# Kernel tuning notes

Hardware: AMD Instinct MI355X
Metric: run time of the kernel (lower is better)

Reference implementation:

```python
import jax, jax.numpy as jnp
import numpy as np

T, B, D, H, O = 512, 64, 1024, 1024, 1024
N_LAYERS = 2


def setup_inputs() -> dict:
    key = jax.random.key(0)
    ks = jax.random.split(key, 1 + 4 * N_LAYERS)
    inp = {
        "x": jax.random.normal(ks[0], (T, B, D), dtype=jnp.float32),
        "paddings": jnp.zeros((T, B, 1), dtype=jnp.float32),
    }
    d_in = D
    for i in range(N_LAYERS):
        s_ih = 1.0 / np.sqrt(d_in)
        s_hh = 1.0 / np.sqrt(H)
        inp[f"Wih{i}"] = jax.random.normal(ks[1 + 4 * i], (d_in, 3 * H), jnp.float32) * s_ih
        inp[f"Whh{i}"] = jax.random.normal(ks[2 + 4 * i], (H, 3 * H), jnp.float32) * s_hh
        inp[f"b{i}"] = jnp.zeros((3 * H,), jnp.float32)
        inp[f"Who{i}"] = jax.random.normal(ks[3 + 4 * i], (H, O), jnp.float32) * s_hh
        d_in = O
    return inp


def _gru_layer(x, p, Wih, Whh, b, Who):
    # x: [T, B, D_in], p: [T, B, 1]
    Bsz = x.shape[1]
    Hd = Whh.shape[0]
    # precompute input-side gates for all steps: [T, B, 3H]
    gx_all = jnp.einsum("tbd,dk->tbk", x, Wih) + b

    def step(h, inp):
        gx, pt = inp  # gx: [B, 3H], pt: [B, 1]
        gh = h @ Whh  # [B, 3H]
        r = jax.nn.sigmoid(gx[:, :Hd] + gh[:, :Hd])
        z = jax.nn.sigmoid(gx[:, Hd:2 * Hd] + gh[:, Hd:2 * Hd])
        n = jnp.tanh(gx[:, 2 * Hd:] + r * gh[:, 2 * Hd:])
        h_new = (1.0 - z) * n + z * h
        h_new = pt * h + (1.0 - pt) * h_new  # padded steps keep state
        return h_new, h_new

    h0 = jnp.zeros((Bsz, Hd), x.dtype)
    _, hs = jax.lax.scan(step, h0, (gx_all, p))  # hs: [T, B, H]
    return jnp.einsum("tbh,ho->tbo", hs, Who)


def reference(x, paddings, Wih0, Whh0, b0, Who0, Wih1, Whh1, b1, Who1):
    layers = [(Wih0, Whh0, b0, Who0), (Wih1, Whh1, b1, Who1)]
    xs = x
    for (Wih, Whh, b, Who) in layers:
        xs = _gru_layer(xs, paddings, Wih, Whh, b, Who)
    return xs
```

## Files before the change

kernel.cpp:

```cpp
#include <hip/hip_runtime.h>
#include <hip/hip_bf16.h>

typedef __bf16 bf16;
typedef __bf16 bf16x8 __attribute__((ext_vector_type(8)));
typedef float  f32x4  __attribute__((ext_vector_type(4)));
typedef unsigned long long u64;
typedef unsigned short u16;

__global__ __launch_bounds__(256) void cast_f32_bf16(const float* __restrict__ in,
                                                     bf16* __restrict__ out) {
    size_t i = ((size_t)blockIdx.x * blockDim.x + threadIdx.x) * 8;
    float4 a = *(const float4*)(in + i);
    float4 b = *(const float4*)(in + i + 4);
    bf16x8 o;
    o[0] = (bf16)a.x; o[1] = (bf16)a.y; o[2] = (bf16)a.z; o[3] = (bf16)a.w;
    o[4] = (bf16)b.x; o[5] = (bf16)b.y; o[6] = (bf16)b.z; o[7] = (bf16)b.w;
    *(bf16x8*)(out + i) = o;
}

__global__ __launch_bounds__(256) void transpose_cast(const float* __restrict__ in,
                                                      bf16* __restrict__ out,
                                                      int R, int C) {
    __shared__ float tile[32][33];
    int c0 = blockIdx.x * 32, r0 = blockIdx.y * 32;
    int tx = threadIdx.x & 31, ty = threadIdx.x >> 5;
    #pragma unroll
    for (int i = 0; i < 32; i += 8)
        tile[ty + i][tx] = in[(size_t)(r0 + ty + i) * C + c0 + tx];
    __syncthreads();
    #pragma unroll
    for (int i = 0; i < 32; i += 8)
        out[(size_t)(c0 + ty + i) * R + r0 + tx] = (bf16)tile[tx][ty + i];
}

template<bool BF16_OUT, bool HAS_BIAS>
__global__ __launch_bounds__(256) void gemm128(const bf16* __restrict__ A,
                                               const bf16* __restrict__ Bt,
                                               const float* __restrict__ bias,
                                               void* __restrict__ Cout,
                                               int M, int N, int K) {
    __shared__ bf16 sA[128][72];
    __shared__ bf16 sB[128][72];
    const int tid = threadIdx.x, lane = tid & 63, w = tid >> 6;
    const int wr = w >> 1, wc = w & 1;
    const int m0 = blockIdx.y * 128, n0 = blockIdx.x * 128;
    const int ml = lane & 15, kb = (lane >> 4) * 8;

    f32x4 acc[4][4] = {};
    const bf16* Ab = A  + (size_t)m0 * K;
    const bf16* Bb = Bt + (size_t)n0 * K;

    for (int kc = 0; kc < K; kc += 64) {
        #pragma unroll
        for (int i = 0; i < 4; ++i) {
            int c = tid + 256 * i;
            int row = c >> 3, col = (c & 7) * 8;
            *(uint4*)&sA[row][col] = *(const uint4*)(Ab + (size_t)row * K + kc + col);
            *(uint4*)&sB[row][col] = *(const uint4*)(Bb + (size_t)row * K + kc + col);
        }
        __syncthreads();
        #pragma unroll
        for (int ks = 0; ks < 2; ++ks) {
            bf16x8 af[4], bfr[4];
            #pragma unroll
            for (int i = 0; i < 4; ++i)
                af[i] = *(const bf16x8*)&sA[wr * 64 + i * 16 + ml][ks * 32 + kb];
            #pragma unroll
            for (int i = 0; i < 4; ++i)
                bfr[i] = *(const bf16x8*)&sB[wc * 64 + i * 16 + ml][ks * 32 + kb];
            #pragma unroll
            for (int mi = 0; mi < 4; ++mi)
                #pragma unroll
                for (int ni = 0; ni < 4; ++ni)
                    acc[mi][ni] = __builtin_amdgcn_mfma_f32_16x16x32_bf16(
                        af[mi], bfr[ni], acc[mi][ni], 0, 0, 0);
        }
        __syncthreads();
    }
    const int rbase = (lane >> 4) * 4;
    #pragma unroll
    for (int mi = 0; mi < 4; ++mi) {
        #pragma unroll
        for (int ni = 0; ni < 4; ++ni) {
            int col = n0 + wc * 64 + ni * 16 + ml;
            float bv = HAS_BIAS ? bias[col] : 0.f;
            #pragma unroll
            for (int r = 0; r < 4; ++r) {
                int row = m0 + wr * 64 + mi * 16 + rbase + r;
                float v = acc[mi][ni][r] + bv;
                if constexpr (BF16_OUT)
                    ((bf16*)Cout)[(size_t)row * N + col] = (bf16)v;
                else
                    ((float*)Cout)[(size_t)row * N + col] = v;
            }
        }
    }
}

__device__ __forceinline__ void mm_step(const char* sW, const char* hslot,
                                        int wv, int lane, int kb, int ml,
                                        f32x4 acc[3]) {
    const char* rowp = hslot + wv * 32768 + (lane >> 4) * 256 + ml * 16;
    uint4 hq[32];
    #pragma unroll
    for (int ks = 0; ks < 32; ++ks)
        asm volatile("global_load_dwordx4 %0, %1, off"
                     : "=v"(hq[ks]) : "v"(rowp + ks * 1024) : "memory");
    asm volatile("s_waitcnt vmcnt(16)" ::: "memory");
    __builtin_amdgcn_sched_barrier(0);
    #pragma unroll
    for (int ks = 0; ks < 16; ++ks) {
        bf16x8 af = __builtin_bit_cast(bf16x8, hq[ks]);
        #pragma unroll
        for (int g = 0; g < 3; ++g) {
            int brow = g * 16 + ml;
            int addr = brow * 2048 + (ks * 32 + kb) * 2;
            addr ^= (brow & 7) << 4;
            bf16x8 bw = *(const bf16x8*)(sW + addr);
            acc[g] = __builtin_amdgcn_mfma_f32_16x16x32_bf16(af, bw, acc[g], 0, 0, 0);
        }
    }
    asm volatile("s_waitcnt vmcnt(0)" ::: "memory");
    __builtin_amdgcn_sched_barrier(0);
    #pragma unroll
    for (int ks = 16; ks < 32; ++ks) {
        bf16x8 af = __builtin_bit_cast(bf16x8, hq[ks]);
        #pragma unroll
        for (int g = 0; g < 3; ++g) {
            int brow = g * 16 + ml;
            int addr = brow * 2048 + (ks * 32 + kb) * 2;
            addr ^= (brow & 7) << 4;
            bf16x8 bw = *(const bf16x8*)(sW + addr);
            acc[g] = __builtin_amdgcn_mfma_f32_16x16x32_bf16(af, bw, acc[g], 0, 0, 0);
        }
    }
}

__device__ __forceinline__ void store_pair_frag(char* slot, int b, int j,
                                                unsigned short v, int ml) {
    unsigned nb = (unsigned)__shfl_xor((int)(unsigned)v, 1, 64);
    if ((ml & 1) == 0) {
        unsigned pk = (unsigned)v | (nb << 16);
        size_t off = (size_t)((b >> 4) * 32768 + (j >> 5) * 1024 +
                              ((j >> 3) & 3) * 256 + (b & 15) * 16 + (j & 7) * 2);
        __hip_atomic_store((unsigned*)(slot + off), pk,
                           __ATOMIC_RELAXED, __HIP_MEMORY_SCOPE_AGENT);
    }
}

__device__ __forceinline__ void poll1(const u16* a, unsigned ta, int lane) {
    while (true) {
        unsigned fa = (unsigned)__hip_atomic_load(a + lane, __ATOMIC_RELAXED,
                                                  __HIP_MEMORY_SCOPE_AGENT);
        if (__all((int)(fa >= ta))) break;
        __builtin_amdgcn_s_sleep(8);
    }
    asm volatile("" ::: "memory");
}

__device__ __forceinline__ void publish1(u16* s1, unsigned val, int lane) {
    asm volatile("s_waitcnt vmcnt(0)" ::: "memory");
    if (lane == 0)
        __hip_atomic_store(s1, (u16)val, __ATOMIC_RELAXED, __HIP_MEMORY_SCOPE_AGENT);
}
__device__ __forceinline__ void publish2(u16* s1, u16* s2, unsigned val, int lane) {
    asm volatile("s_waitcnt vmcnt(0)" ::: "memory");
    if (lane == 0) {
        __hip_atomic_store(s1, (u16)val, __ATOMIC_RELAXED, __HIP_MEMORY_SCOPE_AGENT);
        __hip_atomic_store(s2, (u16)val, __ATOMIC_RELAXED, __HIP_MEMORY_SCOPE_AGENT);
    }
}

__global__ __launch_bounds__(256, 1) void gru_fused(
    const bf16* __restrict__ WH1T, const bf16* __restrict__ W2fT,
    const bf16* __restrict__ WH2T, const bf16* __restrict__ gx1,
    const float* __restrict__ pad, const float* __restrict__ b2,
    char* __restrict__ h1f,
    bf16* __restrict__ gx2ring,
    char* __restrict__ hs2f,
    bf16* __restrict__ hs2row,
    u16* __restrict__ f1s, u16* __restrict__ f1c,
    u16* __restrict__ f2,
    u16* __restrict__ f3s, u16* __restrict__ f3c) {
    extern __shared__ __align__(16) char sW[];

    const int tid = threadIdx.x, lane = tid & 63, wv = tid >> 6;
    const int role = blockIdx.x >> 6, jg = blockIdx.x & 63;
    const int j0 = jg * 16;
    const int ml = lane & 15, kb = (lane >> 4) * 8;
    const int rbase = (lane >> 4) * 4;
    const int bbase = wv * 16 + rbase;
    const int jml = j0 + ml;

    const bf16* Wsrc = (role == 0) ? WH1T : (role == 1) ? W2fT : WH2T;
    #pragma unroll 1
    for (int i = 0; i < 24; ++i) {
        int c = tid + 256 * i;
        int rr = c >> 7;
        int off = (c & 127) * 16;
        int gate = rr >> 4, j = rr & 15;
        const bf16* src = Wsrc + (size_t)(gate * 1024 + j0 + j) * 1024 + off / 2;
        *(uint4*)(sW + rr * 2048 + (off ^ ((rr & 7) << 4))) = *(const uint4*)src;
    }
    __syncthreads();

    if (role == 0) {
        u16* fown = f1s + wv * 64;
        float hreg[4] = {0.f, 0.f, 0.f, 0.f};
        float gxv[12]; float4 pv;
        #pragma unroll
        for (int r = 0; r < 4; ++r) {
            size_t b = (size_t)(bbase + r);
            gxv[r * 3 + 0] = (float)gx1[b * 3072 + jml];
            gxv[r * 3 + 1] = (float)gx1[b * 3072 + 1024 + jml];
            gxv[r * 3 + 2] = (float)gx1[b * 3072 + 2048 + jml];
        }
        pv = *(const float4*)(pad + bbase);

        for (int t = 0; t < 512; ++t) {
            f32x4 acc[3] = {};
            if (t > 0) {
                poll1(fown, (unsigned)t, lane);
                mm_step(sW, h1f + (size_t)(t - 1) * 131072, wv, lane, kb, ml, acc);
            }
            unsigned short hpk[4];
            #pragma unroll
            for (int r = 0; r < 4; ++r) {
                float rr = 1.f / (1.f + __expf(-(gxv[r * 3 + 0] + acc[0][r])));
                float zz = 1.f / (1.f + __expf(-(gxv[r * 3 + 1] + acc[1][r])));
                float nn = tanhf(gxv[r * 3 + 2] + rr * acc[2][r]);
                float hold = hreg[r];
                float hn = (1.f - zz) * nn + zz * hold;
                float p = (r == 0) ? pv.x : (r == 1) ? pv.y : (r == 2) ? pv.z : pv.w;
                hn = p * hold + (1.f - p) * hn;
                hreg[r] = hn;
                hpk[r] = __builtin_bit_cast(unsigned short, (bf16)hn);
            }
            char* hst = h1f + (size_t)t * 131072;
            #pragma unroll
            for (int r = 0; r < 4; ++r)
                store_pair_frag(hst, bbase + r, jml, hpk[r], ml);
            publish2(fown + jg, f1c + wv * 64 + jg, (unsigned)(t + 1), lane);
            {
                int tn = (t < 511) ? t + 1 : 511;
                const bf16* gxt = gx1 + (size_t)tn * 64 * 3072;
                #pragma unroll
                for (int r = 0; r < 4; ++r) {
                    size_t b = (size_t)(bbase + r);
                    gxv[r * 3 + 0] = (float)gxt[b * 3072 + jml];
                    gxv[r * 3 + 1] = (float)gxt[b * 3072 + 1024 + jml];
                    gxv[r * 3 + 2] = (float)gxt[b * 3072 + 2048 + jml];
                }
                pv = *(const float4*)(pad + tn * 64 + bbase);
            }
        }
    } else if (role == 1) {
        u16* fsrc = f1c + wv * 64;
        u16* fbp  = f3c + wv * 64;
        for (int t = 0; t < 512; ++t) {
            poll1(fsrc, (unsigned)(t + 1), lane);
            f32x4 acc[3] = {};
            mm_step(sW, h1f + (size_t)t * 131072, wv, lane, kb, ml, acc);
            if (t >= 16)
                poll1(fbp, (unsigned)(t - 15), lane);
            bf16* dst = gx2ring + (size_t)(t & 15) * 196608;
            #pragma unroll
            for (int g = 0; g < 3; ++g) {
                unsigned short w0 = __builtin_bit_cast(unsigned short, (bf16)acc[g][0]);
                unsigned short w1 = __builtin_bit_cast(unsigned short, (bf16)acc[g][1]);
                unsigned short w2 = __builtin_bit_cast(unsigned short, (bf16)acc[g][2]);
                unsigned short w3 = __builtin_bit_cast(unsigned short, (bf16)acc[g][3]);
                u64 pk = (u64)w0 | ((u64)w1 << 16) | ((u64)w2 << 32) | ((u64)w3 << 48);
                __hip_atomic_store((u64*)(dst + ((size_t)(g * 1024 + jml)) * 64 + bbase),
                                   pk, __ATOMIC_RELAXED, __HIP_MEMORY_SCOPE_AGENT);
            }
            publish1(f2 + wv * 64 + jg, (unsigned)(t + 1), lane);
        }
    } else {
        u16* fown = f3s + wv * 64;
        u16* fgx  = f2 + wv * 64;
        float b2v[3] = {b2[jml], b2[1024 + jml], b2[2048 + jml]};
        float hreg[4] = {0.f, 0.f, 0.f, 0.f};
        float4 pv = *(const float4*)(pad + bbase);

        for (int t = 0; t < 512; ++t) {
            poll1(fgx, (unsigned)(t + 1), lane);
            const bf16* gsl = gx2ring + (size_t)(t & 15) * 196608;
            u64 gq[3];
            #pragma unroll
            for (int g = 0; g < 3; ++g)
                gq[g] = __hip_atomic_load(
                    (const u64*)(gsl + ((size_t)(g * 1024 + jml)) * 64 + bbase),
                    __ATOMIC_RELAXED, __HIP_MEMORY_SCOPE_AGENT);
            f32x4 acc[3] = {};
            if (t > 0) {
                poll1(fown, (unsigned)t, lane);
                mm_step(sW, hs2f + (size_t)((t - 1) & 15) * 131072, wv, lane, kb, ml, acc);
            }
            unsigned short hpk[4];
            #pragma unroll
            for (int r = 0; r < 4; ++r) {
                float gr = (float)__builtin_bit_cast(bf16,
                    (unsigned short)(gq[0] >> (r * 16))) + b2v[0];
                float gz = (float)__builtin_bit_cast(bf16,
                    (unsigned short)(gq[1] >> (r * 16))) + b2v[1];
                float gn = (float)__builtin_bit_cast(bf16,
                    (unsigned short)(gq[2] >> (r * 16))) + b2v[2];
                float rr = 1.f / (1.f + __expf(-(gr + acc[0][r])));
                float zz = 1.f / (1.f + __expf(-(gz + acc[1][r])));
                float nn = tanhf(gn + rr * acc[2][r]);
                float hold = hreg[r];
                float hn = (1.f - zz) * nn + zz * hold;
                float p = (r == 0) ? pv.x : (r == 1) ? pv.y : (r == 2) ? pv.z : pv.w;
                hn = p * hold + (1.f - p) * hn;
                hreg[r] = hn;
                hpk[r] = __builtin_bit_cast(unsigned short, (bf16)hn);
            }
            char* hstf = hs2f + (size_t)(t & 15) * 131072;
            #pragma unroll
            for (int r = 0; r < 4; ++r)
                store_pair_frag(hstf, bbase + r, jml, hpk[r], ml);
            bf16* hstr = hs2row + (size_t)t * 65536;
            #pragma unroll
            for (int r = 0; r < 4; ++r) {
                unsigned nb = (unsigned)__shfl_xor((int)(unsigned)hpk[r], 1, 64);
                if ((ml & 1) == 0) {
                    unsigned pk = (unsigned)hpk[r] | (nb << 16);
                    *(unsigned*)(hstr + (size_t)(bbase + r) * 1024 + jml) = pk;
                }
            }
            publish2(fown + jg, f3c + wv * 64 + jg, (unsigned)(t + 1), lane);
            int tn = (t < 511) ? t + 1 : 511;
            pv = *(const float4*)(pad + tn * 64 + bbase);
        }
    }
}

extern "C" void kernel_launch(void* const* d_in, const int* in_sizes, int n_in,
                              void* d_out, int out_size, void* d_ws, size_t ws_size,
                              hipStream_t stream) {
    const float* x    = (const float*)d_in[0];
    const float* pad  = (const float*)d_in[1];
    const float* Wih1 = (const float*)d_in[2];
    const float* Whh1 = (const float*)d_in[3];
    const float* b1   = (const float*)d_in[4];
    const float* Who1 = (const float*)d_in[5];
    const float* Wih2 = (const float*)d_in[6];
    const float* Whh2 = (const float*)d_in[7];
    const float* b2   = (const float*)d_in[8];
    const float* Who2 = (const float*)d_in[9];
    float* out_f = (float*)d_out;

    char* p = (char*)d_ws;
    bf16* xb      = (bf16*)p; p += (size_t)32768 * 1024 * 2;
    bf16* gxb     = (bf16*)p; p += (size_t)32768 * 3072 * 2;
    char* h1f     = p;        p += (size_t)512 * 131072;
    bf16* hs2row  = (bf16*)p; p += (size_t)32768 * 1024 * 2;
    char* hs2f    = p;        p += (size_t)16 * 131072;
    bf16* gx2ring = (bf16*)p; p += (size_t)16 * 196608 * 2;
    bf16* WT1     = (bf16*)p; p += (size_t)3072 * 1024 * 2;
    bf16* who1b   = (bf16*)p; p += (size_t)1024 * 1024 * 2;
    bf16* W2fT    = (bf16*)p; p += (size_t)3072 * 1024 * 2;
    bf16* WH1     = (bf16*)p; p += (size_t)3072 * 1024 * 2;
    bf16* WH2     = (bf16*)p; p += (size_t)3072 * 1024 * 2;
    u16* flags = (u16*)p; p += 8192;
    u16* f1s = flags,        * f1c = flags + 256;
    u16* f2  = flags + 512;
    u16* f3s = flags + 768,  * f3c = flags + 1024;

    hipFuncSetAttribute((const void*)gru_fused,
                        hipFuncAttributeMaxDynamicSharedMemorySize, 131072);

    cast_f32_bf16<<<16384, 256, 0, stream>>>(x, xb);
    transpose_cast<<<dim3(96, 32), 256, 0, stream>>>(Wih1, WT1, 1024, 3072);
    gemm128<true, true><<<dim3(24, 256), 256, 0, stream>>>(
        xb, WT1, b1, gxb, 32768, 3072, 1024);
    transpose_cast<<<dim3(96, 32), 256, 0, stream>>>(Wih2, WT1, 1024, 3072);
    cast_f32_bf16<<<512, 256, 0, stream>>>(Who1, who1b);
    gemm128<true, false><<<dim3(8, 24), 256, 0, stream>>>(
        WT1, who1b, nullptr, W2fT, 3072, 1024, 1024);
    transpose_cast<<<dim3(96, 32), 256, 0, stream>>>(Whh1, WH1, 1024, 3072);
    transpose_cast<<<dim3(96, 32), 256, 0, stream>>>(Whh2, WH2, 1024, 3072);
    transpose_cast<<<dim3(32, 32), 256, 0, stream>>>(Who2, WT1, 1024, 1024);
    hipMemsetAsync(flags, 0, 8192, stream);
    gru_fused<<<192, 256, 98304, stream>>>(WH1, W2fT, WH2, gxb, pad, b2,
                                           h1f, gx2ring, hs2f, hs2row,
                                           f1s, f1c, f2, f3s, f3c);
    gemm128<false, false><<<dim3(8, 256), 256, 0, stream>>>(
        hs2row, WT1, nullptr, out_f, 32768, 1024, 1024);
}
```

Before: 4.763 ms.

## Split role-1 projection GEMM along K into two halves with wider column tiles

The role-1 blocks, which compute the layer-2 input gates from layer-1 hidden states, now each cover 32 columns over half of K instead of 16 columns over all of K. Each block loads only half of the h slice per step (16 loads instead of 32) and issues 6 MFMA accumulators per k-step, which should shorten per-step latency on the critical pipeline. The two K-halves write separate partial sums into a ring buffer of twice the size, and the role-2 consumer loads both halves and adds them. This doubles gx2 ring traffic and rounds each partial sum to bf16 before the add, which slightly changes precision.

New measurement: 4.950 ms. +3.9%, slower.

```diff
diff --git a/kernel.cpp b/kernel.cpp
--- a/kernel.cpp
+++ b/kernel.cpp
@@ -97,6 +97,7 @@
     }
 }
 
+
 __device__ __forceinline__ void mm_step(const char* sW, const char* hslot,
                                         int wv, int lane, int kb, int ml,
                                         f32x4 acc[3]) {
@@ -133,6 +134,47 @@
             bf16x8 bw = *(const bf16x8*)(sW + addr);
             acc[g] = __builtin_amdgcn_mfma_f32_16x16x32_bf16(af, bw, acc[g], 0, 0, 0);
         }
+    }
+}
+
+__device__ __forceinline__ void mm_step16(const char* sW, const char* hslot,
+                                          int kh, int wv, int lane, int kb, int ml,
+                                          f32x4 acc[3][2]) {
+    const char* rowp = hslot + wv * 32768 + (lane >> 4) * 256 + ml * 16 + kh * 16384;
+    uint4 hq[16];
+    #pragma unroll
+    for (int ks = 0; ks < 16; ++ks)
+        asm volatile("global_load_dwordx4 %0, %1, off"
+                     : "=v"(hq[ks]) : "v"(rowp + ks * 1024) : "memory");
+    asm volatile("s_waitcnt vmcnt(8)" ::: "memory");
+    __builtin_amdgcn_sched_barrier(0);
+    #pragma unroll
+    for (int ks = 0; ks < 8; ++ks) {
+        bf16x8 af = __builtin_bit_cast(bf16x8, hq[ks]);
+        #pragma unroll
+        for (int g = 0; g < 3; ++g)
+            #pragma unroll
+            for (int ct = 0; ct < 2; ++ct) {
+                int brow = g * 32 + ct * 16 + ml;
+                int addr = brow * 1024 + (((ks * 32 + kb) * 2) ^ ((brow & 7) << 4));
+                bf16x8 bw = *(const bf16x8*)(sW + addr);
+                acc[g][ct] = __builtin_amdgcn_mfma_f32_16x16x32_bf16(af, bw, acc[g][ct], 0, 0, 0);
+            }
+    }
+    asm volatile("s_waitcnt vmcnt(0)" ::: "memory");
+    __builtin_amdgcn_sched_barrier(0);
+    #pragma unroll
+    for (int ks = 8; ks < 16; ++ks) {
+        bf16x8 af = __builtin_bit_cast(bf16x8, hq[ks]);
+        #pragma unroll
+        for (int g = 0; g < 3; ++g)
+            #pragma unroll
+            for (int ct = 0; ct < 2; ++ct) {
+                int brow = g * 32 + ct * 16 + ml;
+                int addr = brow * 1024 + (((ks * 32 + kb) * 2) ^ ((brow & 7) << 4));
+                bf16x8 bw = *(const bf16x8*)(sW + addr);
+                acc[g][ct] = __builtin_amdgcn_mfma_f32_16x16x32_bf16(af, bw, acc[g][ct], 0, 0, 0);
+            }
     }
 }
 
@@ -192,15 +234,29 @@
     const int bbase = wv * 16 + rbase;
     const int jml = j0 + ml;
 
-    const bf16* Wsrc = (role == 0) ? WH1T : (role == 1) ? W2fT : WH2T;
-    #pragma unroll 1
-    for (int i = 0; i < 24; ++i) {
-        int c = tid + 256 * i;
-        int rr = c >> 7;
-        int off = (c & 127) * 16;
-        int gate = rr >> 4, j = rr & 15;
-        const bf16* src = Wsrc + (size_t)(gate * 1024 + j0 + j) * 1024 + off / 2;
-        *(uint4*)(sW + rr * 2048 + (off ^ ((rr & 7) << 4))) = *(const uint4*)src;
+    if (role == 1) {
+        const int cgrp = jg >> 1, kh = jg & 1;
+        #pragma unroll 1
+        for (int i = 0; i < 24; ++i) {
+            int c = tid + 256 * i;
+            int row = c >> 6;
+            int off = (c & 63) * 16;
+            int gate = row >> 5, cx = row & 31;
+            const bf16* src = W2fT + (size_t)(gate * 1024 + cgrp * 32 + cx) * 1024
+                              + kh * 512 + off / 2;
+            *(uint4*)(sW + row * 1024 + (off ^ ((row & 7) << 4))) = *(const uint4*)src;
+        }
+    } else {
+        const bf16* Wsrc = (role == 0) ? WH1T : WH2T;
+        #pragma unroll 1
+        for (int i = 0; i < 24; ++i) {
+            int c = tid + 256 * i;
+            int rr = c >> 7;
+            int off = (c & 127) * 16;
+            int gate = rr >> 4, j = rr & 15;
+            const bf16* src = Wsrc + (size_t)(gate * 1024 + j0 + j) * 1024 + off / 2;
+            *(uint4*)(sW + rr * 2048 + (off ^ ((rr & 7) << 4))) = *(const uint4*)src;
+        }
     }
     __syncthreads();
 
@@ -255,25 +311,29 @@
             }
         }
     } else if (role == 1) {
+        const int cgrp = jg >> 1, kh = jg & 1;
         u16* fsrc = f1c + wv * 64;
         u16* fbp  = f3c + wv * 64;
         for (int t = 0; t < 512; ++t) {
             poll1(fsrc, (unsigned)(t + 1), lane);
-            f32x4 acc[3] = {};
-            mm_step(sW, h1f + (size_t)t * 131072, wv, lane, kb, ml, acc);
+            f32x4 acc2[3][2] = {};
+            mm_step16(sW, h1f + (size_t)t * 131072, kh, wv, lane, kb, ml, acc2);
             if (t >= 16)
                 poll1(fbp, (unsigned)(t - 15), lane);
-            bf16* dst = gx2ring + (size_t)(t & 15) * 196608;
-            #pragma unroll
-            for (int g = 0; g < 3; ++g) {
-                unsigned short w0 = __builtin_bit_cast(unsigned short, (bf16)acc[g][0]);
-                unsigned short w1 = __builtin_bit_cast(unsigned short, (bf16)acc[g][1]);
-                unsigned short w2 = __builtin_bit_cast(unsigned short, (bf16)acc[g][2]);
-                unsigned short w3 = __builtin_bit_cast(unsigned short, (bf16)acc[g][3]);
-                u64 pk = (u64)w0 | ((u64)w1 << 16) | ((u64)w2 << 32) | ((u64)w3 << 48);
-                __hip_atomic_store((u64*)(dst + ((size_t)(g * 1024 + jml)) * 64 + bbase),
-                                   pk, __ATOMIC_RELAXED, __HIP_MEMORY_SCOPE_AGENT);
-            }
+            bf16* dst = gx2ring + (size_t)(t & 15) * 393216 + (size_t)kh * 196608;
+            #pragma unroll
+            for (int g = 0; g < 3; ++g)
+                #pragma unroll
+                for (int ct = 0; ct < 2; ++ct) {
+                    int col = cgrp * 32 + ct * 16 + ml;
+                    unsigned short w0 = __builtin_bit_cast(unsigned short, (bf16)acc2[g][ct][0]);
+                    unsigned short w1 = __builtin_bit_cast(unsigned short, (bf16)acc2[g][ct][1]);
+                    unsigned short w2 = __builtin_bit_cast(unsigned short, (bf16)acc2[g][ct][2]);
+                    unsigned short w3 = __builtin_bit_cast(unsigned short, (bf16)acc2[g][ct][3]);
+                    u64 pk = (u64)w0 | ((u64)w1 << 16) | ((u64)w2 << 32) | ((u64)w3 << 48);
+                    __hip_atomic_store((u64*)(dst + ((size_t)(g * 1024 + col)) * 64 + bbase),
+                                       pk, __ATOMIC_RELAXED, __HIP_MEMORY_SCOPE_AGENT);
+                }
             publish1(f2 + wv * 64 + jg, (unsigned)(t + 1), lane);
         }
     } else {
@@ -285,13 +345,16 @@
 
         for (int t = 0; t < 512; ++t) {
             poll1(fgx, (unsigned)(t + 1), lane);
-            const bf16* gsl = gx2ring + (size_t)(t & 15) * 196608;
-            u64 gq[3];
-            #pragma unroll
-            for (int g = 0; g < 3; ++g)
-                gq[g] = __hip_atomic_load(
-                    (const u64*)(gsl + ((size_t)(g * 1024 + jml)) * 64 + bbase),
-                    __ATOMIC_RELAXED, __HIP_MEMORY_SCOPE_AGENT);
+            const bf16* gsl = gx2ring + (size_t)(t & 15) * 393216;
+            u64 gq[2][3];
+            #pragma unroll
+            for (int h = 0; h < 2; ++h)
+                #pragma unroll
+                for (int g = 0; g < 3; ++g)
+                    gq[h][g] = __hip_atomic_load(
+                        (const u64*)(gsl + (size_t)h * 196608 +
+                                     ((size_t)(g * 1024 + jml)) * 64 + bbase),
+                        __ATOMIC_RELAXED, __HIP_MEMORY_SCOPE_AGENT);
             f32x4 acc[3] = {};
             if (t > 0) {
                 poll1(fown, (unsigned)t, lane);
@@ -300,12 +363,15 @@
             unsigned short hpk[4];
             #pragma unroll
             for (int r = 0; r < 4; ++r) {
-                float gr = (float)__builtin_bit_cast(bf16,
-                    (unsigned short)(gq[0] >> (r * 16))) + b2v[0];
-                float gz = (float)__builtin_bit_cast(bf16,
-                    (unsigned short)(gq[1] >> (r * 16))) + b2v[1];
-                float gn = (float)__builtin_bit_cast(bf16,
-                    (unsigned short)(gq[2] >> (r * 16))) + b2v[2];
+                float gr = (float)__builtin_bit_cast(bf16, (unsigned short)(gq[0][0] >> (r * 16)))
+                         + (float)__builtin_bit_cast(bf16, (unsigned short)(gq[1][0] >> (r * 16)))
+                         + b2v[0];
+                float gz = (float)__builtin_bit_cast(bf16, (unsigned short)(gq[0][1] >> (r * 16)))
+                         + (float)__builtin_bit_cast(bf16, (unsigned short)(gq[1][1] >> (r * 16)))
+                         + b2v[1];
+                float gn = (float)__builtin_bit_cast(bf16, (unsigned short)(gq[0][2] >> (r * 16)))
+                         + (float)__builtin_bit_cast(bf16, (unsigned short)(gq[1][2] >> (r * 16)))
+                         + b2v[2];
                 float rr = 1.f / (1.f + __expf(-(gr + acc[0][r])));
                 float zz = 1.f / (1.f + __expf(-(gz + acc[1][r])));
                 float nn = tanhf(gn + rr * acc[2][r]);
@@ -357,7 +423,7 @@
     char* h1f     = p;        p += (size_t)512 * 131072;
     bf16* hs2row  = (bf16*)p; p += (size_t)32768 * 1024 * 2;
     char* hs2f    = p;        p += (size_t)16 * 131072;
-    bf16* gx2ring = (bf16*)p; p += (size_t)16 * 196608 * 2;
+    bf16* gx2ring = (bf16*)p; p += (size_t)16 * 393216 * 2;
     bf16* WT1     = (bf16*)p; p += (size_t)3072 * 1024 * 2;
     bf16* who1b   = (bf16*)p; p += (size_t)1024 * 1024 * 2;
     bf16* W2fT    = (bf16*)p; p += (size_t)3072 * 1024 * 2;
```
